# Performance work log

Hardware: AMD Instinct MI355X
Metric: run time of the kernel (lower is better)

Reference implementation:

```python
import jax, jax.numpy as jnp
import numpy as np

B, N = 4, 2466  # batch, vertex count (Pixel2Mesh stage-3 mesh)
IMG = 224.0


def _vertex_align(feat_maps, pos):
    """Bilinear-style gather of image features at projected vertex locations.
    feat_maps: list of [B,C,S,S]; pos: [B,N,3]. Returns [B,N,sum(C)]."""
    z = pos[..., 2]
    h = jnp.clip(248.0 * (pos[..., 1] / z) + 111.5, 0.0, 223.0)
    w = jnp.clip(248.0 * (pos[..., 0] / (-z)) + 111.5, 0.0, 223.0)
    outs = []
    for f in feat_maps:
        S = f.shape[-1]
        x = h / (IMG / S)
        y = w / (IMG / S)
        x1 = jnp.floor(x).astype(jnp.int32)
        x2 = jnp.minimum(jnp.ceil(x).astype(jnp.int32), S - 1)
        y1 = jnp.floor(y).astype(jnp.int32)
        y2 = jnp.minimum(jnp.ceil(y).astype(jnp.int32), S - 1)
        xi = x.astype(jnp.int32)  # trunc == floor since x >= 0
        yi = y.astype(jnp.int32)

        def gat(fm, xs, ys):  # fm [C,S,S], xs/ys [N] -> [N,C]
            return fm[:, xs, ys].T

        g = jax.vmap(gat)
        w11 = ((x2 - xi) * (y2 - yi)).astype(f.dtype)[..., None]
        w12 = ((x2 - xi) * (yi - y1)).astype(f.dtype)[..., None]
        w21 = ((xi - x1) * (y2 - yi)).astype(f.dtype)[..., None]
        w22 = ((xi - x1) * (yi - y1)).astype(f.dtype)[..., None]
        outs.append(w11 * g(f, x1, y1) + w21 * g(f, x2, y1)
                    + w12 * g(f, x1, y2) + w22 * g(f, x2, y2))
    return jnp.concatenate(outs, axis=-1)


def _graph_conv(x, adj, w0, w1):
    # relu(X @ w0 + A @ (X @ w1))
    return jax.nn.relu(x @ w0 + jnp.einsum('bmn,bnc->bmc', adj, x @ w1))


def _res_graph_conv(x, adj, pw, pb, w00, w01, w10, w11):
    skip = x @ pw + pb
    out = _graph_conv(x, adj, w00, w01)
    out = _graph_conv(out, adj, w10, w11)
    return skip + out


def _forward(conv2_3, conv3_4, conv4_6, conv5_3, vertex_positions, vertex_features,
             vertex_adjacency, lin_w, lin_b,
             r0_pw, r0_pb, r0_w00, r0_w01, r0_w10, r0_w11,
             r1_pw, r1_pb, r1_w00, r1_w01, r1_w10, r1_w11,
             r2_pw, r2_pb, r2_w00, r2_w01, r2_w10, r2_w11,
             gf_w0, gf_w1):
    aligned = _vertex_align([conv2_3, conv3_4, conv4_6, conv5_3], vertex_positions)  # [B,N,3840]
    proj = aligned @ lin_w + lin_b  # [B,N,128]
    x = jnp.concatenate([proj, vertex_features, vertex_positions], axis=-1)  # [B,N,259]
    x = _res_graph_conv(x, vertex_adjacency, r0_pw, r0_pb, r0_w00, r0_w01, r0_w10, r0_w11)
    x = _res_graph_conv(x, vertex_adjacency, r1_pw, r1_pb, r1_w00, r1_w01, r1_w10, r1_w11)
    x = _res_graph_conv(x, vertex_adjacency, r2_pw, r2_pb, r2_w00, r2_w01, r2_w10, r2_w11)
    offset = jnp.tanh(_graph_conv(x, vertex_adjacency, gf_w0, gf_w1))  # [B,N,3]
    return vertex_positions + offset


def setup_inputs() -> dict:
    key = jax.random.key(0)
    ks = jax.random.split(key, 40)
    inp = {
        "conv2_3": jax.random.normal(ks[0], (B, 256, 56, 56), jnp.float32),
        "conv3_4": jax.random.normal(ks[1], (B, 512, 28, 28), jnp.float32),
        "conv4_6": jax.random.normal(ks[2], (B, 1024, 14, 14), jnp.float32),
        "conv5_3": jax.random.normal(ks[3], (B, 2048, 7, 7), jnp.float32),
        "vertex_positions": jax.random.normal(ks[4], (B, N, 3), jnp.float32),
        "vertex_features": jax.random.normal(ks[5], (B, N, 128), jnp.float32),
        # sparse 0/1 adjacency stored dense (the torch module uses dense bmm)
        "vertex_adjacency": (jax.random.uniform(ks[6], (B, N, N)) < 0.003).astype(jnp.float32),
    }

    def u(k, shape, fan):
        b = 1.0 / np.sqrt(fan)
        return jax.random.uniform(k, shape, jnp.float32, -b, b)

    specs = [("lin_w", (3840, 128), 3840), ("lin_b", (128,), 3840)]
    for j, ci in enumerate([259, 128, 128]):
        p = f"r{j}_"
        specs += [(p + "pw", (ci, 128), ci), (p + "pb", (128,), ci),
                  (p + "w00", (ci, 128), ci), (p + "w01", (ci, 128), ci),
                  (p + "w10", (128, 128), 128), (p + "w11", (128, 128), 128)]
    specs += [("gf_w0", (128, 3), 128), ("gf_w1", (128, 3), 128)]
    for i, (name, shape, fan) in enumerate(specs):
        inp[name] = u(ks[7 + i], shape, fan)
    return inp


def reference(conv2_3, conv3_4, conv4_6, conv5_3, vertex_positions, vertex_features,
              vertex_adjacency, lin_w, lin_b,
              r0_pw, r0_pb, r0_w00, r0_w01, r0_w10, r0_w11,
              r1_pw, r1_pb, r1_w00, r1_w01, r1_w10, r1_w11,
              r2_pw, r2_pb, r2_w00, r2_w01, r2_w10, r2_w11,
              gf_w0, gf_w1):
    return _forward(conv2_3, conv3_4, conv4_6, conv5_3, vertex_positions, vertex_features,
                    vertex_adjacency, lin_w, lin_b,
                    r0_pw, r0_pb, r0_w00, r0_w01, r0_w10, r0_w11,
                    r1_pw, r1_pb, r1_w00, r1_w01, r1_w10, r1_w11,
                    r2_pw, r2_pb, r2_w00, r2_w01, r2_w10, r2_w11,
                    gf_w0, gf_w1)
```

## Files before the change

### kernel.cpp

```cpp
#include <hip/hip_runtime.h>
#include <cmath>

#define B_   4
#define N_   2466
#define R_   (B_*N_)
#define ELLW 96
#define NMT  624
#define PARTF ((size_t)NMT * 2048)

typedef _Float16 f16x8 __attribute__((ext_vector_type(8)));
typedef _Float16 f16x4 __attribute__((ext_vector_type(4)));
typedef __attribute__((ext_vector_type(4))) float f32x4;

__device__ __forceinline__ unsigned short f16_bits(float x) {
  union { _Float16 h; unsigned short u; } c;
  c.h = (_Float16)x;
  return c.u;
}
__device__ __forceinline__ float f16_val(unsigned short u) {
  union { unsigned short u; _Float16 h; } c;
  c.u = u;
  return (float)c.h;
}

struct WMats { const float* p[15]; };


__global__ __launch_bounds__(256) void k_pre(
    const float* __restrict__ c2, const float* __restrict__ c3,
    const float* __restrict__ c4, const float* __restrict__ c5,
    unsigned short* __restrict__ t0, unsigned short* __restrict__ t1,
    unsigned short* __restrict__ t2, unsigned short* __restrict__ t3,
    const float* __restrict__ adj, int* __restrict__ cols, int* __restrict__ cnts,
    const float* __restrict__ lin_w,
    unsigned short* __restrict__ whf,
    WMats wm,
    unsigned short* __restrict__ wrf) {
  __shared__ float t[64][66];
  int bid = blockIdx.x;
  int tid = threadIdx.x;
  if (bid < 1584) {
    const float* in; unsigned short* out; int C, P, npb, ncb, rem;
    if (bid < 784)       { in = c2; out = t0; C = 256;  P = 3136; npb = 49; ncb = 4;  rem = bid; }
    else if (bid < 1200) { in = c3; out = t1; C = 512;  P = 784;  npb = 13; ncb = 8;  rem = bid - 784; }
    else if (bid < 1456) { in = c4; out = t2; C = 1024; P = 196;  npb = 4;  ncb = 16; rem = bid - 1200; }
    else                 { in = c5; out = t3; C = 2048; P = 49;   npb = 1;  ncb = 32; rem = bid - 1456; }
    int pb = rem % npb; int tq = rem / npb; int cb = tq % ncb; int b = tq / ncb;
    int c0 = cb * 64, p0 = pb * 64;
    #pragma unroll
    for (int i = 0; i < 8; i++) {
      int e = tid + i * 256;
      int c = e >> 5, f2 = e & 31;
      int p = p0 + f2 * 2;
      float2 v = make_float2(0.f, 0.f);
      const float* src = in + ((size_t)b * C + (c0 + c)) * P + p;
      if (p + 1 < P)      v = *(const float2*)src;
      else if (p < P)     v.x = *src;
      *(float2*)&t[c][f2 * 2] = v;
    }
    __syncthreads();
    int jj = tid & 15, c4i = jj * 4;
    #pragma unroll
    for (int pass = 0; pass < 4; pass++) {
      int pp = pass * 16 + (tid >> 4);
      int px = p0 + pp;
      if (px < P) {
        ushort4 o;
        o.x = f16_bits(t[c4i + 0][pp]);
        o.y = f16_bits(t[c4i + 1][pp]);
        o.z = f16_bits(t[c4i + 2][pp]);
        o.w = f16_bits(t[c4i + 3][pp]);
        *(ushort4*)&out[((size_t)b * P + px) * C + c0 + c4i] = o;
      }
    }
  } else if (bid < 11448) {
    int row = bid - 1584;
    int wv = tid >> 6, lane = tid & 63;
    const float* Ar = adj + (size_t)row * N_;
    int* cp = cols + (size_t)row * ELLW;
    unsigned long long below = (lane == 63) ? 0xFFFFFFFFFFFFFFFFull >> 1
                                            : ((1ull << lane) - 1ull);
    int jbeg = wv * 640;
    int jend = (jbeg + 640 < N_) ? jbeg + 640 : N_;
    unsigned long long m[3][4];
    int cnt = 0;
    #pragma unroll
    for (int i = 0; i < 3; i++) {
      int j0 = jbeg + i * 256 + lane * 4;
      float4 v = make_float4(0.f, 0.f, 0.f, 0.f);
      if (j0 + 3 < jend) {
        v = *(const float4*)&Ar[j0];
      } else {
        if (j0     < jend) v.x = Ar[j0];
        if (j0 + 1 < jend) v.y = Ar[j0+1];
        if (j0 + 2 < jend) v.z = Ar[j0+2];
      }
      m[i][0] = __ballot((j0     < jend) && (v.x != 0.f));
      m[i][1] = __ballot((j0 + 1 < jend) && (v.y != 0.f));
      m[i][2] = __ballot((j0 + 2 < jend) && (v.z != 0.f));
      m[i][3] = __ballot((j0 + 3 < jend) && (v.w != 0.f));
      cnt += __popcll(m[i][0]) + __popcll(m[i][1])
           + __popcll(m[i][2]) + __popcll(m[i][3]);
    }
    int* sc = (int*)&t[0][0];
    if (lane == 0) sc[wv] = cnt;
    __syncthreads();
    int base = 0;
    #pragma unroll
    for (int w2 = 0; w2 < 4; w2++) {
      int c = sc[w2];
      if (w2 < wv) base += c;
    }
    int tot = sc[0] + sc[1] + sc[2] + sc[3];
    int run = base;
    #pragma unroll
    for (int i = 0; i < 3; i++) {
      int j0 = jbeg + i * 256 + lane * 4;
      unsigned long long m0 = m[i][0], m1 = m[i][1], m2 = m[i][2], m3 = m[i][3];
      int pre = __popcll(m0 & below) + __popcll(m1 & below)
              + __popcll(m2 & below) + __popcll(m3 & below);
      bool nz0 = (m0 >> lane) & 1ull;
      bool nz1 = (m1 >> lane) & 1ull;
      bool nz2 = (m2 >> lane) & 1ull;
      bool nz3 = (m3 >> lane) & 1ull;
      int p0 = run + pre;
      int p1 = p0 + (nz0 ? 1 : 0);
      int p2 = p1 + (nz1 ? 1 : 0);
      int p3 = p2 + (nz2 ? 1 : 0);
      if (nz0 && p0 < ELLW) cp[p0] = j0;
      if (nz1 && p1 < ELLW) cp[p1] = j0 + 1;
      if (nz2 && p2 < ELLW) cp[p2] = j0 + 2;
      if (nz3 && p3 < ELLW) cp[p3] = j0 + 3;
      run += __popcll(m0) + __popcll(m1) + __popcll(m2) + __popcll(m3);
    }
    if (wv == 3 && lane == 0) cnts[row] = (tot > ELLW) ? ELLW : tot;
  } else if (bid < 11928) {
    int b = bid - 11448;
    int e0 = (b * 256 + tid) * 4;
    #pragma unroll
    for (int u = 0; u < 4; u++) {
      int e = e0 + u;
      int j = e & 7;
      int lane = (e >> 3) & 63;
      int nt = (e >> 9) & 7;
      int slab = e >> 12;
      int k = slab * 32 + ((lane >> 4) << 3) + j;
      int n = nt * 16 + (lane & 15);
      whf[e] = f16_bits(lin_w[(size_t)k * 128 + n]);
    }
  } else {
    int b = bid - 11928;
    int e0 = (b * 256 + tid) * 4;
    #pragma unroll
    for (int u = 0; u < 4; u++) {
      int e = e0 + u;
      int rb, mat, rem, K;
      if (e < 143360) {
        rb = 0;
        if (e < 110592) { mat = e / 36864; rem = e - mat * 36864; K = 259; }
        else { int tt = e - 110592; mat = 3 + tt / 16384; rem = tt & 16383; K = 128; }
      } else {
        int tt = e - 143360;
        rb = 1 + tt / 81920;
        int r2 = tt % 81920;
        mat = r2 / 16384; rem = r2 & 16383; K = 128;
      }
      int j = rem & 7, lane = (rem >> 3) & 63, nt = (rem >> 9) & 7, slab = rem >> 12;
      int k = slab * 32 + ((lane >> 4) << 3) + j;
      int n = nt * 16 + (lane & 15);
      float x = (k < K) ? wm.p[rb * 5 + mat][(size_t)k * 128 + n] : 0.f;
      wrf[e] = f16_bits(x);
    }
  }
}

__global__ __launch_bounds__(256) void k_align_mfma(
    const unsigned short* __restrict__ tr0, const unsigned short* __restrict__ tr1,
    const unsigned short* __restrict__ tr2, const unsigned short* __restrict__ tr3,
    const float* __restrict__ pos,
    const unsigned short* __restrict__ whf,
    unsigned short* __restrict__ part, int kchunk) {
  int tid  = threadIdx.x;
  int wave = tid >> 6, lane = tid & 63;
  int q    = lane >> 4, l15 = lane & 15;
  int m0   = blockIdx.x * 128;
  int s    = blockIdx.y;

  int zero[2][4]; int base[2][4];
  #pragma unroll
  for (int u = 0; u < 2; u++) {
    int mrow = m0 + (wave * 2 + u) * 16 + l15;
    int rowc = (mrow < R_) ? mrow : 0;
    int b = rowc / N_;
    float px = pos[rowc*3+0], py = pos[rowc*3+1], pz = pos[rowc*3+2];
    float hh = fminf(fmaxf(248.f*(py/pz)    + 111.5f, 0.f), 223.f);
    float wc = fminf(fmaxf(248.f*(px/(-pz)) + 111.5f, 0.f), 223.f);
    const int Sarr[4] = {56, 28, 14, 7};
    const int Carr[4] = {256, 512, 1024, 2048};
    #pragma unroll
    for (int sc = 0; sc < 4; sc++) {
      int S = Sarr[sc], C = Carr[sc];
      float dv = 224.f / (float)S;
      float x = hh / dv, y = wc / dv;
      int x1 = (int)floorf(x), y1 = (int)floorf(y);
      int x2 = min((int)ceilf(x), S - 1), y2 = min((int)ceilf(y), S - 1);
      int w = (x2 - x1) * (y2 - y1);
      zero[u][sc] = (mrow >= R_) || (w == 0);
      base[u][sc] = (b * S * S + x1 * S + y1) * C;
    }
  }

  f32x4 acc[2][8];
  #pragma unroll
  for (int u = 0; u < 2; u++)
    #pragma unroll
    for (int nt = 0; nt < 8; nt++) acc[u][nt] = (f32x4){0.f, 0.f, 0.f, 0.f};

  const f16x8* BH = (const f16x8*)whf;

  int kbeg = s * kchunk, kend = kbeg + kchunk;
  #pragma unroll 1
  for (int k0 = kbeg; k0 < kend; k0 += 32) {
    const unsigned short* tr; int off, sI;
    if (k0 < 256)       { tr = tr0; off = 0;    sI = 0; }
    else if (k0 < 768)  { tr = tr1; off = 256;  sI = 1; }
    else if (k0 < 1792) { tr = tr2; off = 768;  sI = 2; }
    else                { tr = tr3; off = 1792; sI = 3; }

    f16x8 af[2];
    #pragma unroll
    for (int u = 0; u < 2; u++) {
      af[u] = *(const f16x8*)(tr + base[u][sI] + (k0 - off) + q * 8);
      if (zero[u][sI]) af[u] = (f16x8)(_Float16)0;
    }

    int slab = k0 >> 5;
    f16x8 Bh[8];
    #pragma unroll
    for (int nt = 0; nt < 8; nt++)
      Bh[nt] = BH[(size_t)(slab * 8 + nt) * 64 + lane];
    #pragma unroll
    for (int nt = 0; nt < 8; nt++) {
      acc[0][nt] = __builtin_amdgcn_mfma_f32_16x16x32_f16(af[0], Bh[nt], acc[0][nt], 0, 0, 0);
      acc[1][nt] = __builtin_amdgcn_mfma_f32_16x16x32_f16(af[1], Bh[nt], acc[1][nt], 0, 0, 0);
    }
  }

  #pragma unroll
  for (int u = 0; u < 2; u++) {
    int mt = blockIdx.x * 8 + wave * 2 + u;
    int row0 = mt * 16 + q * 4;
    #pragma unroll
    for (int nt = 0; nt < 8; nt++) {
      if (row0 < R_) {
        ushort4 ov;
        ov.x = f16_bits(acc[u][nt][0]);
        ov.y = f16_bits(acc[u][nt][1]);
        ov.z = f16_bits(acc[u][nt][2]);
        ov.w = f16_bits(acc[u][nt][3]);
        *(ushort4*)&part[(((size_t)s * NMT + mt) * 8 + nt) * 256 + lane * 4] = ov;
      }
    }
  }
}

__global__ __launch_bounds__(256) void k_xgemm(
    const unsigned short* __restrict__ part, const float* __restrict__ lin_b,
    const float* __restrict__ vf, const float* __restrict__ pos, int nsplit,
    const unsigned short* __restrict__ wf, const float* __restrict__ pb,
    unsigned short* __restrict__ o0, unsigned short* __restrict__ o1,
    unsigned short* __restrict__ o2) {
  __shared__ unsigned short hsm[16][296];
  int tid = threadIdx.x;
  int r0 = blockIdx.x * 16;
  int mt = blockIdx.x;
  int wave = tid >> 6, lane = tid & 63;

  {
    int l15 = lane & 15, qq = lane >> 4;
    #pragma unroll
    for (int nt2 = 0; nt2 < 2; nt2++) {
      int nt = wave * 2 + nt2;
      int col = nt * 16 + l15;
      float b = lin_b[col];
      float a4[4] = {b, b, b, b};
      for (int s = 0; s < nsplit; s++) {
        ushort4 pv = *(const ushort4*)&part[(((size_t)s * NMT + mt) * 8 + nt) * 256 + lane * 4];
        a4[0] += f16_val(pv.x); a4[1] += f16_val(pv.y);
        a4[2] += f16_val(pv.z); a4[3] += f16_val(pv.w);
      }
      #pragma unroll
      for (int r = 0; r < 4; r++)
        hsm[qq * 4 + r][col] = f16_bits(a4[r]);
    }
  }
  {
    int grp = tid >> 5, ln = tid & 31;
    #pragma unroll
    for (int rr = 0; rr < 2; rr++) {
      int lrow = grp * 2 + rr;
      int row = r0 + lrow;
      int rowc = (row < R_) ? row : (R_ - 1);
      float4 vv = ((const float4*)vf)[(size_t)rowc * 32 + ln];
      ushort4 o;
      o.x = f16_bits(vv.x); o.y = f16_bits(vv.y);
      o.z = f16_bits(vv.z); o.w = f16_bits(vv.w);
      *(ushort4*)&hsm[lrow][128 + ln * 4] = o;
      if (ln < 8) {
        ushort4 z = make_ushort4(0, 0, 0, 0);
        if (ln == 0) {
          z.x = f16_bits(pos[(size_t)rowc * 3 + 0]);
          z.y = f16_bits(pos[(size_t)rowc * 3 + 1]);
          z.z = f16_bits(pos[(size_t)rowc * 3 + 2]);
        }
        *(ushort4*)&hsm[lrow][256 + ln * 4] = z;
      }
    }
  }
  __syncthreads();

  int q = lane >> 4, l15 = lane & 15;
  const unsigned short* xrow = &hsm[l15][q * 8];

  #pragma unroll 1
  for (int which = 0; which < 3; which++) {
    const f16x8* BH = (const f16x8*)(wf + (size_t)which * 36864);
    f32x4 acc[2];
    #pragma unroll
    for (int t2 = 0; t2 < 2; t2++) acc[t2] = (f32x4){0.f, 0.f, 0.f, 0.f};
    #pragma unroll
    for (int slab = 0; slab < 9; slab++) {
      f16x8 af = *(const f16x8*)(xrow + slab * 32);
      f16x8 Bh[2];
      #pragma unroll
      for (int t2 = 0; t2 < 2; t2++)
        Bh[t2] = BH[(size_t)(slab * 8 + wave * 2 + t2) * 64 + lane];
      #pragma unroll
      for (int t2 = 0; t2 < 2; t2++)
        acc[t2] = __builtin_amdgcn_mfma_f32_16x16x32_f16(af, Bh[t2], acc[t2], 0, 0, 0);
    }
    unsigned short* out = (which == 0) ? o0 : (which == 1) ? o1 : o2;
    #pragma unroll
    for (int t2 = 0; t2 < 2; t2++) {
      int col = (wave * 2 + t2) * 16 + l15;
      float bias = (which == 2) ? pb[col] : 0.f;
      #pragma unroll
      for (int r = 0; r < 4; r++) {
        int row = r0 + q * 4 + r;
        if (row < R_) out[(size_t)row * 128 + col] = f16_bits(acc[t2][r] + bias);
      }
    }
  }
}

template<int NW>
__global__ __launch_bounds__(256) void k_fuse(
    const unsigned short* __restrict__ s_in,
    const unsigned short* __restrict__ t_in,
    const unsigned short* __restrict__ skip_in,
    const int* __restrict__ cols, const int* __restrict__ cnts,
    const unsigned short* __restrict__ wf, const float* __restrict__ pb,
    unsigned short* __restrict__ o0, unsigned short* __restrict__ o1,
    unsigned short* __restrict__ o2) {
  __shared__ unsigned short hsm[16][136];
  int tid = threadIdx.x;
  int r0 = blockIdx.x * 16;

  {
    int grp = tid >> 5, ln = tid & 31;
    const f16x4* s4 = (const f16x4*)s_in;
    const f16x4* t4 = (const f16x4*)t_in;
    #pragma unroll 1
    for (int rr = 0; rr < 2; rr++) {
      int lrow = grp * 2 + rr;
      int row = r0 + lrow;
      int rowc = (row < R_) ? row : (R_ - 1);
      int b = rowc / N_;
      size_t tbase = (size_t)b * N_;
      const int* cp = cols + (size_t)rowc * ELLW;
      int4 ci0 = *(const int4*)cp;
      int4 ci1 = *(const int4*)(cp + 4);
      int4 ci2 = *(const int4*)(cp + 8);
      int cnt = cnts[rowc];
      f16x4 sv = s4[(size_t)rowc*32 + ln];
      float4 acc = make_float4((float)sv[0], (float)sv[1], (float)sv[2], (float)sv[3]);
      int idx[12] = {ci0.x, ci0.y, ci0.z, ci0.w, ci1.x, ci1.y, ci1.z, ci1.w,
                     ci2.x, ci2.y, ci2.z, ci2.w};
      f16x4 g[12];
      #pragma unroll
      for (int i = 0; i < 12; i++) {
        int c = idx[i];
        c = (c >= 0 && c < N_) ? c : 0;
        g[i] = t4[(tbase + c)*32 + ln];
      }
      #pragma unroll
      for (int i = 0; i < 12; i++) {
        if (i < cnt) {
          acc.x += (float)g[i][0]; acc.y += (float)g[i][1];
          acc.z += (float)g[i][2]; acc.w += (float)g[i][3];
        }
      }
      for (int i = 12; i < cnt; i++) {
        f16x4 v = t4[(tbase + cp[i])*32 + ln];
        acc.x += (float)v[0]; acc.y += (float)v[1];
        acc.z += (float)v[2]; acc.w += (float)v[3];
      }
      acc.x = fmaxf(acc.x, 0.f); acc.y = fmaxf(acc.y, 0.f);
      acc.z = fmaxf(acc.z, 0.f); acc.w = fmaxf(acc.w, 0.f);
      if (skip_in) {
        f16x4 sk = ((const f16x4*)skip_in)[(size_t)rowc*32 + ln];
        acc.x += (float)sk[0]; acc.y += (float)sk[1];
        acc.z += (float)sk[2]; acc.w += (float)sk[3];
      }
      ushort4 o;
      o.x = f16_bits(acc.x); o.y = f16_bits(acc.y);
      o.z = f16_bits(acc.z); o.w = f16_bits(acc.w);
      *(ushort4*)&hsm[lrow][ln * 4] = o;
    }
  }
  __syncthreads();

  int wave = tid >> 6, lane = tid & 63;
  int q = lane >> 4, l15 = lane & 15;
  const unsigned short* xrow = &hsm[l15][q * 8];

  #pragma unroll 1
  for (int which = 0; which < NW; which++) {
    const f16x8* BH = (const f16x8*)(wf + (size_t)which * 16384);
    f32x4 acc[2];
    #pragma unroll
    for (int t2 = 0; t2 < 2; t2++) acc[t2] = (f32x4){0.f, 0.f, 0.f, 0.f};
    #pragma unroll
    for (int slab = 0; slab < 4; slab++) {
      f16x8 af = *(const f16x8*)(xrow + slab * 32);
      f16x8 Bh[2];
      #pragma unroll
      for (int t2 = 0; t2 < 2; t2++)
        Bh[t2] = BH[(size_t)(slab * 8 + wave * 2 + t2) * 64 + lane];
      #pragma unroll
      for (int t2 = 0; t2 < 2; t2++)
        acc[t2] = __builtin_amdgcn_mfma_f32_16x16x32_f16(af, Bh[t2], acc[t2], 0, 0, 0);
    }
    unsigned short* out = (which == 0) ? o0 : (which == 1) ? o1 : o2;
    #pragma unroll
    for (int t2 = 0; t2 < 2; t2++) {
      int col = (wave * 2 + t2) * 16 + l15;
      float bias = (pb != nullptr && which == 2) ? pb[col] : 0.f;
      #pragma unroll
      for (int r = 0; r < 4; r++) {
        int row = r0 + q * 4 + r;
        if (row < R_) out[(size_t)row * 128 + col] = f16_bits(acc[t2][r] + bias);
      }
    }
  }
}

__global__ __launch_bounds__(256) void k_spmm(
    const unsigned short* __restrict__ sb, const unsigned short* __restrict__ tb,
    const int* __restrict__ cols, const int* __restrict__ cnts,
    const unsigned short* __restrict__ skipb, unsigned short* __restrict__ outb,
    const float* __restrict__ gw0, const float* __restrict__ gw1,
    unsigned short* __restrict__ gsb, unsigned short* __restrict__ gtb, int fuse_gf) {
  int tid = threadIdx.x;
  int grp = tid >> 5, ln = tid & 31;
  int row = blockIdx.x * 8 + grp;
  int b = row / N_;
  size_t tbase = (size_t)b * N_;
  const f16x4* sb4 = (const f16x4*)sb;
  const f16x4* tb4 = (const f16x4*)tb;
  const int* cp = cols + (size_t)row * ELLW;
  int4 ci0 = *(const int4*)cp;
  int4 ci1 = *(const int4*)(cp + 4);
  int4 ci2 = *(const int4*)(cp + 8);
  int cnt = cnts[row];
  f16x4 sv = sb4[(size_t)row*32 + ln];
  float4 acc = make_float4((float)sv[0], (float)sv[1], (float)sv[2], (float)sv[3]);
  int idx[12] = {ci0.x, ci0.y, ci0.z, ci0.w, ci1.x, ci1.y, ci1.z, ci1.w,
                 ci2.x, ci2.y, ci2.z, ci2.w};
  f16x4 g[12];
  #pragma unroll
  for (int i = 0; i < 12; i++) {
    int c = idx[i];
    c = (c >= 0 && c < N_) ? c : 0;
    g[i] = tb4[(tbase + c)*32 + ln];
  }
  #pragma unroll
  for (int i = 0; i < 12; i++) {
    if (i < cnt) {
      acc.x += (float)g[i][0]; acc.y += (float)g[i][1];
      acc.z += (float)g[i][2]; acc.w += (float)g[i][3];
    }
  }
  for (int i = 12; i < cnt; i++) {
    f16x4 v = tb4[(tbase + cp[i])*32 + ln];
    acc.x += (float)v[0]; acc.y += (float)v[1];
    acc.z += (float)v[2]; acc.w += (float)v[3];
  }
  acc.x = fmaxf(acc.x, 0.f); acc.y = fmaxf(acc.y, 0.f);
  acc.z = fmaxf(acc.z, 0.f); acc.w = fmaxf(acc.w, 0.f);
  if (skipb) {
    f16x4 sk = ((const f16x4*)skipb)[(size_t)row*32 + ln];
    acc.x += (float)sk[0]; acc.y += (float)sk[1];
    acc.z += (float)sk[2]; acc.w += (float)sk[3];
  }
  if (!fuse_gf) {
    ushort4 o;
    o.x = f16_bits(acc.x); o.y = f16_bits(acc.y);
    o.z = f16_bits(acc.z); o.w = f16_bits(acc.w);
    ((ushort4*)outb)[(size_t)row*32 + ln] = o;
    return;
  }
  float av[4] = {acc.x, acc.y, acc.z, acc.w};
  int j0 = ln * 4;
  float p0 = 0.f, p1 = 0.f, p2 = 0.f, q0 = 0.f, q1 = 0.f, q2 = 0.f;
  #pragma unroll
  for (int u = 0; u < 4; u++) {
    int j = j0 + u;
    p0 += av[u] * gw0[j*3+0]; p1 += av[u] * gw0[j*3+1]; p2 += av[u] * gw0[j*3+2];
    q0 += av[u] * gw1[j*3+0]; q1 += av[u] * gw1[j*3+1]; q2 += av[u] * gw1[j*3+2];
  }
  #pragma unroll
  for (int off = 16; off >= 1; off >>= 1) {
    p0 += __shfl_xor(p0, off); p1 += __shfl_xor(p1, off); p2 += __shfl_xor(p2, off);
    q0 += __shfl_xor(q0, off); q1 += __shfl_xor(q1, off); q2 += __shfl_xor(q2, off);
  }
  if (ln == 0) {
    gsb[(size_t)row*4 + 0] = f16_bits(p0);
    gsb[(size_t)row*4 + 1] = f16_bits(p1);
    gsb[(size_t)row*4 + 2] = f16_bits(p2);
    gtb[(size_t)row*4 + 0] = f16_bits(q0);
    gtb[(size_t)row*4 + 1] = f16_bits(q1);
    gtb[(size_t)row*4 + 2] = f16_bits(q2);
  }
}

__global__ __launch_bounds__(256) void k_gf_final(
    const unsigned short* __restrict__ sb, const unsigned short* __restrict__ tb,
    const int* __restrict__ cols, const int* __restrict__ cnts,
    const float* __restrict__ pos, float* __restrict__ out) {
  int wave = threadIdx.x >> 6, lane = threadIdx.x & 63;
  int row = blockIdx.x * 4 + wave;
  if (lane >= 3) return;
  int b = row / N_;
  size_t tbase = (size_t)b * N_;
  const int* cp = cols + (size_t)row * ELLW;
  int4 ci0 = *(const int4*)cp;
  int4 ci1 = *(const int4*)(cp + 4);
  int4 ci2 = *(const int4*)(cp + 8);
  int cnt = cnts[row];
  float acc = f16_val(sb[(size_t)row*4 + lane]);
  int idx[12] = {ci0.x, ci0.y, ci0.z, ci0.w, ci1.x, ci1.y, ci1.z, ci1.w,
                 ci2.x, ci2.y, ci2.z, ci2.w};
  float g[12];
  #pragma unroll
  for (int i = 0; i < 12; i++) {
    int c = idx[i];
    c = (c >= 0 && c < N_) ? c : 0;
    g[i] = f16_val(tb[(tbase + c)*4 + lane]);
  }
  #pragma unroll
  for (int i = 0; i < 12; i++)
    if (i < cnt) acc += g[i];
  for (int i = 12; i < cnt; i++) {
    acc += f16_val(tb[(tbase + cp[i])*4 + lane]);
  }
  float v = tanhf(fmaxf(acc, 0.f));
  out[(size_t)row*3 + lane] = pos[(size_t)row*3 + lane] + v;
}

extern "C" void kernel_launch(void* const* d_in, const int* in_sizes, int n_in,
                              void* d_out, int out_size, void* d_ws, size_t ws_size,
                              hipStream_t stream) {
  const float* conv2_3 = (const float*)d_in[0];
  const float* conv3_4 = (const float*)d_in[1];
  const float* conv4_6 = (const float*)d_in[2];
  const float* conv5_3 = (const float*)d_in[3];
  const float* pos     = (const float*)d_in[4];
  const float* vf      = (const float*)d_in[5];
  const float* adj     = (const float*)d_in[6];
  const float* lin_w   = (const float*)d_in[7];
  const float* lin_b   = (const float*)d_in[8];
  const float* r_pb[3]  = {(const float*)d_in[10], (const float*)d_in[16], (const float*)d_in[22]};
  const float* gf_w0 = (const float*)d_in[27];
  const float* gf_w1 = (const float*)d_in[28];
  float* out = (float*)d_out;

  const size_t ROWF    = (size_t)R_ * 128;
  const size_t LINW_E  = 491520;
  const size_t RESW_E  = 307200;

  unsigned short* trh0 = (unsigned short*)d_ws;
  unsigned short* trh1 = trh0 + (size_t)4*256*3136;
  unsigned short* trh2 = trh1 + (size_t)4*512*784;
  unsigned short* trh3 = trh2 + (size_t)4*1024*196;
  int*   ell_cnt  = (int*)(trh3 + (size_t)4*2048*49);
  int*   ell_cols = ell_cnt + R_;
  unsigned short* whf = (unsigned short*)(ell_cols + (size_t)R_*ELLW);
  unsigned short* wrf = whf + LINW_E;
  unsigned short* part = wrf + RESW_E + 512;

  size_t fixed_h = 6021120 + 2*(size_t)R_*(ELLW+1) + LINW_E + RESW_E + 512;
  size_t need8 = (fixed_h + (size_t)8*PARTF + 8*ROWF + 1024) * 2;
  int nsplit = (ws_size >= need8) ? 8 : 4;
  int kchunk = 3840 / nsplit;

  unsigned short* sb   = part + (size_t)nsplit * PARTF;
  unsigned short* tb   = sb   + ROWF;
  unsigned short* sb2  = tb   + ROWF;
  unsigned short* tb2  = sb2  + ROWF;
  unsigned short* skA  = tb2  + ROWF;
  unsigned short* skB  = skA  + ROWF;
  unsigned short* gsb  = skB  + ROWF;
  unsigned short* gtb  = gsb  + (size_t)R_ * 4;

  WMats wm;
  for (int rb = 0; rb < 3; rb++) {
    wm.p[rb*5 + 0] = (const float*)d_in[11 + 6*rb];
    wm.p[rb*5 + 1] = (const float*)d_in[12 + 6*rb];
    wm.p[rb*5 + 2] = (const float*)d_in[9  + 6*rb];
    wm.p[rb*5 + 3] = (const float*)d_in[13 + 6*rb];
    wm.p[rb*5 + 4] = (const float*)d_in[14 + 6*rb];
  }

  const int NFB = (R_ + 15) / 16;

  k_pre<<<12228, 256, 0, stream>>>(conv2_3, conv3_4, conv4_6, conv5_3,
                                   trh0, trh1, trh2, trh3,
                                   adj, ell_cols, ell_cnt,
                                   lin_w, whf, wm, wrf);

  k_align_mfma<<<dim3(78, nsplit), 256, 0, stream>>>(trh0, trh1, trh2, trh3, pos,
                                                     whf, part, kchunk);

  k_xgemm<<<NFB, 256, 0, stream>>>(part, lin_b, vf, pos, nsplit,
                                   wrf + 0, r_pb[0], sb, tb, skA);

  k_fuse<2><<<NFB, 256, 0, stream>>>(sb, tb, nullptr, ell_cols, ell_cnt,
                                     wrf + 110592, nullptr, sb2, tb2, nullptr);

  k_fuse<3><<<NFB, 256, 0, stream>>>(sb2, tb2, skA, ell_cols, ell_cnt,
                                     wrf + 143360, r_pb[1], sb, tb, skB);

  k_fuse<2><<<NFB, 256, 0, stream>>>(sb, tb, nullptr, ell_cols, ell_cnt,
                                     wrf + 192512, nullptr, sb2, tb2, nullptr);

  k_fuse<3><<<NFB, 256, 0, stream>>>(sb2, tb2, skB, ell_cols, ell_cnt,
                                     wrf + 225280, r_pb[2], sb, tb, skA);

  k_fuse<2><<<NFB, 256, 0, stream>>>(sb, tb, nullptr, ell_cols, ell_cnt,
                                     wrf + 274432, nullptr, sb2, tb2, nullptr);

  k_spmm<<<1233, 256, 0, stream>>>(sb2, tb2, ell_cols, ell_cnt, skA, nullptr,
                                   gf_w0, gf_w1, gsb, gtb, 1);

  k_gf_final<<<2466, 256, 0, stream>>>(gsb, gtb, ell_cols, ell_cnt, pos, out);
}
```

Baseline: 345.0 us.

## Overlap adjacency ELL build and weight conversion with the align GEMM

Splits the preprocessing kernel in two. Feature-map transposes and lin_w conversion stay in the first kernel. The adjacency-to-ELL scan and the residual weight conversion move into the same launch as the vertex-align MFMA GEMM, with align blocks dispatched first. The aim is to run the bandwidth-heavy dense adjacency scan alongside the low-occupancy align GEMM (78*nsplit blocks) instead of serialising them. The fused kernel may compete for memory bandwidth and register or occupancy budget between the heterogeneous block types.

```diff
diff --git a/kernel.cpp b/kernel.cpp
--- a/kernel.cpp
+++ b/kernel.cpp
@@ -26,16 +26,12 @@
 struct WMats { const float* p[15]; };
 
 
-__global__ __launch_bounds__(256) void k_pre(
+__global__ __launch_bounds__(256) void k_preA(
     const float* __restrict__ c2, const float* __restrict__ c3,
     const float* __restrict__ c4, const float* __restrict__ c5,
     unsigned short* __restrict__ t0, unsigned short* __restrict__ t1,
     unsigned short* __restrict__ t2, unsigned short* __restrict__ t3,
-    const float* __restrict__ adj, int* __restrict__ cols, int* __restrict__ cnts,
-    const float* __restrict__ lin_w,
-    unsigned short* __restrict__ whf,
-    WMats wm,
-    unsigned short* __restrict__ wrf) {
+    const float* __restrict__ lin_w, unsigned short* __restrict__ whf) {
   __shared__ float t[64][66];
   int bid = blockIdx.x;
   int tid = threadIdx.x;
@@ -73,8 +69,120 @@
         *(ushort4*)&out[((size_t)b * P + px) * C + c0 + c4i] = o;
       }
     }
-  } else if (bid < 11448) {
-    int row = bid - 1584;
+  } else {
+    int b = bid - 1584;
+    int e0 = (b * 256 + tid) * 4;
+    #pragma unroll
+    for (int u = 0; u < 4; u++) {
+      int e = e0 + u;
+      int j = e & 7;
+      int lane = (e >> 3) & 63;
+      int nt = (e >> 9) & 7;
+      int slab = e >> 12;
+      int k = slab * 32 + ((lane >> 4) << 3) + j;
+      int n = nt * 16 + (lane & 15);
+      whf[e] = f16_bits(lin_w[(size_t)k * 128 + n]);
+    }
+  }
+}
+
+__global__ __launch_bounds__(256) void k_alignB(
+    const unsigned short* __restrict__ tr0, const unsigned short* __restrict__ tr1,
+    const unsigned short* __restrict__ tr2, const unsigned short* __restrict__ tr3,
+    const float* __restrict__ pos,
+    const unsigned short* __restrict__ whf,
+    unsigned short* __restrict__ part, int kchunk, int algnN,
+    const float* __restrict__ adj, int* __restrict__ cols, int* __restrict__ cnts,
+    WMats wm, unsigned short* __restrict__ wrf) {
+  __shared__ int sc[4];
+  int bid = blockIdx.x;
+  int tid = threadIdx.x;
+
+  if (bid < algnN) {
+    int wave = tid >> 6, lane = tid & 63;
+    int q    = lane >> 4, l15 = lane & 15;
+    int bx   = bid % 78;
+    int s    = bid / 78;
+    int m0   = bx * 128;
+
+    int zero[2][4]; int base[2][4];
+    #pragma unroll
+    for (int u = 0; u < 2; u++) {
+      int mrow = m0 + (wave * 2 + u) * 16 + l15;
+      int rowc = (mrow < R_) ? mrow : 0;
+      int b = rowc / N_;
+      float px = pos[rowc*3+0], py = pos[rowc*3+1], pz = pos[rowc*3+2];
+      float hh = fminf(fmaxf(248.f*(py/pz)    + 111.5f, 0.f), 223.f);
+      float wc = fminf(fmaxf(248.f*(px/(-pz)) + 111.5f, 0.f), 223.f);
+      const int Sarr[4] = {56, 28, 14, 7};
+      const int Carr[4] = {256, 512, 1024, 2048};
+      #pragma unroll
+      for (int scI = 0; scI < 4; scI++) {
+        int S = Sarr[scI], C = Carr[scI];
+        float dv = 224.f / (float)S;
+        float x = hh / dv, y = wc / dv;
+        int x1 = (int)floorf(x), y1 = (int)floorf(y);
+        int x2 = min((int)ceilf(x), S - 1), y2 = min((int)ceilf(y), S - 1);
+        int w = (x2 - x1) * (y2 - y1);
+        zero[u][scI] = (mrow >= R_) || (w == 0);
+        base[u][scI] = (b * S * S + x1 * S + y1) * C;
+      }
+    }
+
+    f32x4 acc[2][8];
+    #pragma unroll
+    for (int u = 0; u < 2; u++)
+      #pragma unroll
+      for (int nt = 0; nt < 8; nt++) acc[u][nt] = (f32x4){0.f, 0.f, 0.f, 0.f};
+
+    const f16x8* BH = (const f16x8*)whf;
+
+    int kbeg = s * kchunk, kend = kbeg + kchunk;
+    #pragma unroll 1
+    for (int k0 = kbeg; k0 < kend; k0 += 32) {
+      const unsigned short* tr; int off, sI;
+      if (k0 < 256)       { tr = tr0; off = 0;    sI = 0; }
+      else if (k0 < 768)  { tr = tr1; off = 256;  sI = 1; }
+      else if (k0 < 1792) { tr = tr2; off = 768;  sI = 2; }
+      else                { tr = tr3; off = 1792; sI = 3; }
+
+      f16x8 af[2];
+      #pragma unroll
+      for (int u = 0; u < 2; u++) {
+        af[u] = *(const f16x8*)(tr + base[u][sI] + (k0 - off) + q * 8);
+        if (zero[u][sI]) af[u] = (f16x8)(_Float16)0;
+      }
+
+      int slab = k0 >> 5;
+      f16x8 Bh[8];
+      #pragma unroll
+      for (int nt = 0; nt < 8; nt++)
+        Bh[nt] = BH[(size_t)(slab * 8 + nt) * 64 + lane];
+      #pragma unroll
+      for (int nt = 0; nt < 8; nt++) {
+        acc[0][nt] = __builtin_amdgcn_mfma_f32_16x16x32_f16(af[0], Bh[nt], acc[0][nt], 0, 0, 0);
+        acc[1][nt] = __builtin_amdgcn_mfma_f32_16x16x32_f16(af[1], Bh[nt], acc[1][nt], 0, 0, 0);
+      }
+    }
+
+    #pragma unroll
+    for (int u = 0; u < 2; u++) {
+      int mt = bx * 8 + wave * 2 + u;
+      int row0 = mt * 16 + q * 4;
+      #pragma unroll
+      for (int nt = 0; nt < 8; nt++) {
+        if (row0 < R_) {
+          ushort4 ov;
+          ov.x = f16_bits(acc[u][nt][0]);
+          ov.y = f16_bits(acc[u][nt][1]);
+          ov.z = f16_bits(acc[u][nt][2]);
+          ov.w = f16_bits(acc[u][nt][3]);
+          *(ushort4*)&part[(((size_t)s * NMT + mt) * 8 + nt) * 256 + lane * 4] = ov;
+        }
+      }
+    }
+  } else if (bid < algnN + R_) {
+    int row = bid - algnN;
     int wv = tid >> 6, lane = tid & 63;
     const float* Ar = adj + (size_t)row * N_;
     int* cp = cols + (size_t)row * ELLW;
@@ -102,7 +210,6 @@
       cnt += __popcll(m[i][0]) + __popcll(m[i][1])
            + __popcll(m[i][2]) + __popcll(m[i][3]);
     }
-    int* sc = (int*)&t[0][0];
     if (lane == 0) sc[wv] = cnt;
     __syncthreads();
     int base = 0;
@@ -134,22 +241,8 @@
       run += __popcll(m0) + __popcll(m1) + __popcll(m2) + __popcll(m3);
     }
     if (wv == 3 && lane == 0) cnts[row] = (tot > ELLW) ? ELLW : tot;
-  } else if (bid < 11928) {
-    int b = bid - 11448;
-    int e0 = (b * 256 + tid) * 4;
-    #pragma unroll
-    for (int u = 0; u < 4; u++) {
-      int e = e0 + u;
-      int j = e & 7;
-      int lane = (e >> 3) & 63;
-      int nt = (e >> 9) & 7;
-      int slab = e >> 12;
-      int k = slab * 32 + ((lane >> 4) << 3) + j;
-      int n = nt * 16 + (lane & 15);
-      whf[e] = f16_bits(lin_w[(size_t)k * 128 + n]);
-    }
   } else {
-    int b = bid - 11928;
+    int b = bid - (algnN + R_);
     int e0 = (b * 256 + tid) * 4;
     #pragma unroll
     for (int u = 0; u < 4; u++) {
@@ -170,96 +263,6 @@
       int n = nt * 16 + (lane & 15);
       float x = (k < K) ? wm.p[rb * 5 + mat][(size_t)k * 128 + n] : 0.f;
       wrf[e] = f16_bits(x);
-    }
-  }
-}
-
-__global__ __launch_bounds__(256) void k_align_mfma(
-    const unsigned short* __restrict__ tr0, const unsigned short* __restrict__ tr1,
-    const unsigned short* __restrict__ tr2, const unsigned short* __restrict__ tr3,
-    const float* __restrict__ pos,
-    const unsigned short* __restrict__ whf,
-    unsigned short* __restrict__ part, int kchunk) {
-  int tid  = threadIdx.x;
-  int wave = tid >> 6, lane = tid & 63;
-  int q    = lane >> 4, l15 = lane & 15;
-  int m0   = blockIdx.x * 128;
-  int s    = blockIdx.y;
-
-  int zero[2][4]; int base[2][4];
-  #pragma unroll
-  for (int u = 0; u < 2; u++) {
-    int mrow = m0 + (wave * 2 + u) * 16 + l15;
-    int rowc = (mrow < R_) ? mrow : 0;
-    int b = rowc / N_;
-    float px = pos[rowc*3+0], py = pos[rowc*3+1], pz = pos[rowc*3+2];
-    float hh = fminf(fmaxf(248.f*(py/pz)    + 111.5f, 0.f), 223.f);
-    float wc = fminf(fmaxf(248.f*(px/(-pz)) + 111.5f, 0.f), 223.f);
-    const int Sarr[4] = {56, 28, 14, 7};
-    const int Carr[4] = {256, 512, 1024, 2048};
-    #pragma unroll
-    for (int sc = 0; sc < 4; sc++) {
-      int S = Sarr[sc], C = Carr[sc];
-      float dv = 224.f / (float)S;
-      float x = hh / dv, y = wc / dv;
-      int x1 = (int)floorf(x), y1 = (int)floorf(y);
-      int x2 = min((int)ceilf(x), S - 1), y2 = min((int)ceilf(y), S - 1);
-      int w = (x2 - x1) * (y2 - y1);
-      zero[u][sc] = (mrow >= R_) || (w == 0);
-      base[u][sc] = (b * S * S + x1 * S + y1) * C;
-    }
-  }
-
-  f32x4 acc[2][8];
-  #pragma unroll
-  for (int u = 0; u < 2; u++)
-    #pragma unroll
-    for (int nt = 0; nt < 8; nt++) acc[u][nt] = (f32x4){0.f, 0.f, 0.f, 0.f};
-
-  const f16x8* BH = (const f16x8*)whf;
-
-  int kbeg = s * kchunk, kend = kbeg + kchunk;
-  #pragma unroll 1
-  for (int k0 = kbeg; k0 < kend; k0 += 32) {
-    const unsigned short* tr; int off, sI;
-    if (k0 < 256)       { tr = tr0; off = 0;    sI = 0; }
-    else if (k0 < 768)  { tr = tr1; off = 256;  sI = 1; }
-    else if (k0 < 1792) { tr = tr2; off = 768;  sI = 2; }
-    else                { tr = tr3; off = 1792; sI = 3; }
-
-    f16x8 af[2];
-    #pragma unroll
-    for (int u = 0; u < 2; u++) {
-      af[u] = *(const f16x8*)(tr + base[u][sI] + (k0 - off) + q * 8);
-      if (zero[u][sI]) af[u] = (f16x8)(_Float16)0;
-    }
-
-    int slab = k0 >> 5;
-    f16x8 Bh[8];
-    #pragma unroll
-    for (int nt = 0; nt < 8; nt++)
-      Bh[nt] = BH[(size_t)(slab * 8 + nt) * 64 + lane];
-    #pragma unroll
-    for (int nt = 0; nt < 8; nt++) {
-      acc[0][nt] = __builtin_amdgcn_mfma_f32_16x16x32_f16(af[0], Bh[nt], acc[0][nt], 0, 0, 0);
-      acc[1][nt] = __builtin_amdgcn_mfma_f32_16x16x32_f16(af[1], Bh[nt], acc[1][nt], 0, 0, 0);
-    }
-  }
-
-  #pragma unroll
-  for (int u = 0; u < 2; u++) {
-    int mt = blockIdx.x * 8 + wave * 2 + u;
-    int row0 = mt * 16 + q * 4;
-    #pragma unroll
-    for (int nt = 0; nt < 8; nt++) {
-      if (row0 < R_) {
-        ushort4 ov;
-        ov.x = f16_bits(acc[u][nt][0]);
-        ov.y = f16_bits(acc[u][nt][1]);
-        ov.z = f16_bits(acc[u][nt][2]);
-        ov.w = f16_bits(acc[u][nt][3]);
-        *(ushort4*)&part[(((size_t)s * NMT + mt) * 8 + nt) * 256 + lane * 4] = ov;
-      }
     }
   }
 }
@@ -603,6 +606,7 @@
   size_t need8 = (fixed_h + (size_t)8*PARTF + 8*ROWF + 1024) * 2;
   int nsplit = (ws_size >= need8) ? 8 : 4;
   int kchunk = 3840 / nsplit;
+  int algnN  = 78 * nsplit;
 
   unsigned short* sb   = part + (size_t)nsplit * PARTF;
   unsigned short* tb   = sb   + ROWF;
@@ -624,13 +628,12 @@
 
   const int NFB = (R_ + 15) / 16;
 
-  k_pre<<<12228, 256, 0, stream>>>(conv2_3, conv3_4, conv4_6, conv5_3,
-                                   trh0, trh1, trh2, trh3,
-                                   adj, ell_cols, ell_cnt,
-                                   lin_w, whf, wm, wrf);
-
-  k_align_mfma<<<dim3(78, nsplit), 256, 0, stream>>>(trh0, trh1, trh2, trh3, pos,
-                                                     whf, part, kchunk);
+  k_preA<<<2064, 256, 0, stream>>>(conv2_3, conv3_4, conv4_6, conv5_3,
+                                   trh0, trh1, trh2, trh3, lin_w, whf);
+
+  k_alignB<<<algnN + R_ + 300, 256, 0, stream>>>(trh0, trh1, trh2, trh3, pos,
+                                                 whf, part, kchunk, algnN,
+                                                 adj, ell_cols, ell_cnt, wm, wrf);
 
   k_xgemm<<<NFB, 256, 0, stream>>>(part, lin_b, vf, pos, nsplit,
                                    wrf + 0, r_pb[0], sb, tb, skA);
```

Result: slower. 358.0 us (+3.7%).
